# Performance work log

Measured on AMD Instinct MI355X. Metric: run time of the kernel, lower is better.

## Reference

```python
import jax, jax.numpy as jnp
import numpy as np

S = 100        # sos_token_num
H = 12         # num heads
LY = 3         # number of residual blocks
NEG = -100.0   # attention-bias masking value


def layer_norm(x, w, b, eps=1e-5):
    u = jnp.mean(x, -1, keepdims=True)
    v = jnp.mean((x - u) ** 2, -1, keepdims=True)
    return (x - u) / jnp.sqrt(v + eps) * w + b


def quick_gelu(x):
    return x * jax.nn.sigmoid(1.702 * x)


def l2norm(x, eps=1e-12):
    return x / jnp.maximum(jnp.linalg.norm(x, axis=-1, keepdims=True), eps)


def setup_inputs() -> dict:
    key = jax.random.key(0)
    ks = iter(jax.random.split(key, 32))
    n, c, hh, ww, out_dim = 2, 768, 32, 32, 512
    r = lambda shape, s=1.0: jax.random.normal(next(ks), shape, jnp.float32) * s
    return dict(
        cls_token=r((1, n, c)),
        pix_feat=r((n, c, hh, ww)),
        last_surgery=r((1 + hh * ww, n, c)),
        attn_bias=r((n, 1, S, hh, ww)),
        qkv_w=r((LY, 3 * c, c), 0.02), qkv_b=jnp.zeros((LY, 3 * c)),
        proj_w=r((LY, c, c), 0.02), proj_b=jnp.zeros((LY, c)),
        ln1_w=jnp.ones((LY, c)), ln1_b=jnp.zeros((LY, c)),
        ln2_w=jnp.ones((LY, c)), ln2_b=jnp.zeros((LY, c)),
        fc_w=r((LY, 4 * c, c), 0.02), fc_b=jnp.zeros((LY, 4 * c)),
        fc2_w=r((LY, c, 4 * c), 0.02), fc2_b=jnp.zeros((LY, c)),
        lnp_w=jnp.ones((c,)), lnp_b=jnp.zeros((c,)),
        proj_out=r((c, out_dim), 0.02),
    )


def reference(cls_token, pix_feat, last_surgery, attn_bias,
              qkv_w, qkv_b, proj_w, proj_b,
              ln1_w, ln1_b, ln2_w, ln2_b,
              fc_w, fc_b, fc2_w, fc2_b,
              lnp_w, lnp_b, proj_out):
    n, c, hh, ww = pix_feat.shape
    L = hh * ww
    N = S + 1 + L
    d = c // H
    scale = d ** -0.5

    # ---- assemble token streams (batch-first [n, N, c]) ----
    pix_tok = pix_feat.reshape(n, c, L).transpose(2, 0, 1)          # [L, n, c]
    x = jnp.concatenate([jnp.broadcast_to(cls_token, (S, n, c)), cls_token, pix_tok], 0)
    x_sur = jnp.concatenate([jnp.broadcast_to(last_surgery[0:1], (S, n, c)), last_surgery], 0)
    xo = x.transpose(1, 0, 2)      # 'original' stream  [n, N, c]
    xs = x_sur.transpose(1, 0, 2)  # 'surgery'  stream  [n, N, c]

    # ---- build attention biases (identity downsample: bias already at (h, w)) ----
    base = jnp.zeros((N, N), jnp.float32)
    base = base.at[:, :S].set(NEG)
    base = base.at[jnp.arange(S), jnp.arange(S)].set(0.0)
    base = base.at[:S, S].set(NEG)
    plain = jnp.broadcast_to(base, (n, H, N, N))
    bias = jnp.broadcast_to(attn_bias, (n, H, S, hh, ww)).reshape(n, H, S, L)
    biased = plain.at[:, :, :S, S + 1:].set(bias)   # sos rows attend to pixels via bias

    def attention(t, l):
        # t: [n, N, c] (post-ln_1); returns (surgery_res, ori_res)
        qkv = (t @ qkv_w[l].T + qkv_b[l]).reshape(n, N, 3, H, d).transpose(2, 0, 3, 1, 4)
        q, k, v = qkv[0], qkv[1], qkv[2]   # each [n, H, N, d]
        def attend(q_, k_, mask):
            a = jax.nn.softmax(jnp.einsum('bhnd,bhmd->bhnm', q_, k_) * scale + mask, axis=-1)
            o = jnp.einsum('bhnm,bhmd->bhnd', a, v).transpose(0, 2, 1, 3).reshape(n, N, c)
            return o @ proj_w[l].T + proj_b[l]
        x_ori_res = attend(q, k, biased)   # standard pass, biased mask (attn_mask[0])
        x_res = attend(v, v, plain)        # q = k = v surgery pass (attn_mask[1])
        return x_res, x_ori_res

    for l in range(LY):
        t = layer_norm(xo, ln1_w[l], ln1_b[l])
        res_sur, res_ori = attention(t, l)
        xo = xo + res_ori
        xo = xo + (quick_gelu(layer_norm(xo, ln2_w[l], ln2_b[l]) @ fc_w[l].T + fc_b[l]) @ fc2_w[l].T + fc2_b[l])
        xs = xs + res_sur

    # ---- heads ----
    sos = l2norm(layer_norm(xo[:, :S], lnp_w, lnp_b) @ proj_out)          # [n, S, out]
    img = l2norm(layer_norm(xs[:, S:], lnp_w, lnp_b) @ proj_out)          # [n, 1+L, out]
    img = img[:, 1:, :].transpose(0, 2, 1).reshape(n, proj_out.shape[1], hh, ww)
    return sos, img
```

## Files before the change

### kernel.cpp

```cpp
#include <hip/hip_runtime.h>
#include <math.h>


constexpr int Cc = 768;
constexpr int Ss = 100;
constexpr int Hh = 12;
constexpr int Ll = 1024;
constexpr int Nn = 1125;
constexpr int NB = 2;

typedef unsigned short u16;
typedef __attribute__((ext_vector_type(8))) short short8v;
typedef __attribute__((ext_vector_type(8))) unsigned short ushort8v;
typedef __attribute__((ext_vector_type(4))) float f32x4;

__device__ inline u16 f2bf(float f) {
  unsigned u = __builtin_bit_cast(unsigned int, f);
  unsigned r = u + 0x7fffu + ((u >> 16) & 1u);
  return (u16)(r >> 16);
}
__device__ inline float bf2f(u16 v) {
  return __builtin_bit_cast(float, (unsigned int)v << 16);
}

__device__ inline int swz(int row, int col) {
  return (row << 6) + ((((col >> 3) ^ (row & 7)) << 3) | (col & 7));
}

__global__ __launch_bounds__(256) void assemble_kernel(
    const float* __restrict__ cls, const float* __restrict__ pix,
    const float* __restrict__ sur, float* __restrict__ xo, float* __restrict__ xs) {
  int idx = blockIdx.x * 256 + (int)threadIdx.x;
  int total = NB * Nn * Cc;
  if (idx >= total) return;
  int ch = idx % Cc;
  int t  = (idx / Cc) % Nn;
  int b  = idx / (Cc * Nn);
  float vo, vs;
  if (t <= Ss) vo = cls[b * Cc + ch];
  else         vo = pix[(size_t)b * Cc * Ll + (size_t)ch * Ll + (t - Ss - 1)];
  if (t < Ss)  vs = sur[b * Cc + ch];
  else         vs = sur[(size_t)(t - Ss) * NB * Cc + b * Cc + ch];
  xo[idx] = vo;
  xs[idx] = vs;
}

constexpr int CN0 = 3 * 2304 * 768;
constexpr int CN1 = 3 * 768 * 768;
constexpr int CN2 = 3 * 3072 * 768;
constexpr int CN3 = 3 * 768 * 3072;
__global__ __launch_bounds__(256) void cvt4_kernel(
    const float* __restrict__ s0, const float* __restrict__ s1,
    const float* __restrict__ s2, const float* __restrict__ s3,
    u16* __restrict__ dst) {
  int i4 = (blockIdx.x * 256 + (int)threadIdx.x) * 4;
  if (i4 >= CN0 + CN1 + CN2 + CN3) return;
  const float* src; int off;
  if (i4 < CN0)             { src = s0; off = i4; }
  else if (i4 < CN0 + CN1)  { src = s1; off = i4 - CN0; }
  else if (i4 < CN0 + CN1 + CN2) { src = s2; off = i4 - CN0 - CN1; }
  else                      { src = s3; off = i4 - CN0 - CN1 - CN2; }
  float4 v = *(const float4*)(src + off);
  *(ushort4*)(dst + i4) = make_ushort4(f2bf(v.x), f2bf(v.y), f2bf(v.z), f2bf(v.w));
}

__global__ __launch_bounds__(256) void transpose_po_kernel(
    const float* __restrict__ in, u16* __restrict__ out) {
  int id = blockIdx.x * 256 + (int)threadIdx.x;
  if (id >= 512 * 768) return;
  int nidx = id / 768, k = id - nidx * 768;
  out[id] = f2bf(in[(size_t)k * 512 + nidx]);
}

__global__ __launch_bounds__(256) void ln_kernel(
    const float* __restrict__ X, const float* __restrict__ w, const float* __restrict__ b,
    u16* __restrict__ Y, int rows_per_b, int row_off) {
  int r = blockIdx.x;
  int bb = r / rows_per_b;
  int i  = r % rows_per_b;
  const float* x = X + ((size_t)bb * Nn + row_off + i) * Cc;
  u16* y = Y + (size_t)r * Cc;
  int tid = (int)threadIdx.x;
  float v0 = x[tid], v1 = x[tid + 256], v2 = x[tid + 512];
  float s = v0 + v1 + v2;
  __shared__ float sbuf[4];
  for (int off = 32; off; off >>= 1) s += __shfl_xor(s, off);
  if ((tid & 63) == 0) sbuf[tid >> 6] = s;
  __syncthreads();
  float mean = (sbuf[0] + sbuf[1] + sbuf[2] + sbuf[3]) * (1.0f / Cc);
  float d0 = v0 - mean, d1 = v1 - mean, d2 = v2 - mean;
  float q = d0 * d0 + d1 * d1 + d2 * d2;
  __syncthreads();
  for (int off = 32; off; off >>= 1) q += __shfl_xor(q, off);
  if ((tid & 63) == 0) sbuf[tid >> 6] = q;
  __syncthreads();
  float var = (sbuf[0] + sbuf[1] + sbuf[2] + sbuf[3]) * (1.0f / Cc);
  float inv = rsqrtf(var + 1e-5f);
  y[tid]       = f2bf(d0 * inv * w[tid]       + b[tid]);
  y[tid + 256] = f2bf(d1 * inv * w[tid + 256] + b[tid + 256]);
  y[tid + 512] = f2bf(d2 * inv * w[tid + 512] + b[tid + 512]);
}

__global__ __launch_bounds__(256) void gemm64_kernel(
    const u16* __restrict__ A0, const u16* __restrict__ A1,
    const u16* __restrict__ B, const float* __restrict__ bias,
    const float* __restrict__ res0, const float* __restrict__ res1,
    float* __restrict__ outf0, float* __restrict__ outf1,
    u16* __restrict__ outb0, u16* __restrict__ outb1,
    int M, int N, int K, int act) {
  __shared__ __align__(16) u16 Als[64 * 64];
  __shared__ __align__(16) u16 Bls[128 * 64];
  int zz = blockIdx.z;
  const u16* A = zz ? A1 : A0;
  const float* res = zz ? res1 : res0;
  float* outf = zz ? outf1 : outf0;
  u16* outb = zz ? outb1 : outb0;
  int tid = (int)threadIdx.x;
  int wave = tid >> 6, lane = tid & 63, g = lane >> 4, li = lane & 15;
  int row0 = blockIdx.y * 64, col0 = blockIdx.x * 128;

  const u16* aptr[2]; int dA[2];
#pragma unroll
  for (int j = 0; j < 2; ++j) {
    int ca = tid + j * 256;
    int r = ca >> 3, c8 = ca & 7;
    dA[j] = (r << 6) + ((c8 ^ (r & 7)) << 3);
    int ra = row0 + r; if (ra > M - 1) ra = M - 1;
    aptr[j] = A + (size_t)ra * K + (c8 << 3);
  }
  const u16* bptr[4]; int dB[4];
#pragma unroll
  for (int j = 0; j < 4; ++j) {
    int cb = tid + j * 256;
    int r = cb >> 3, c8 = cb & 7;
    dB[j] = (r << 6) + ((c8 ^ (r & 7)) << 3);
    bptr[j] = B + (size_t)(col0 + r) * K + (c8 << 3);
  }

  f32x4 acc[4][2];
#pragma unroll
  for (int mi = 0; mi < 4; ++mi)
#pragma unroll
    for (int ni = 0; ni < 2; ++ni) acc[mi][ni] = (f32x4){0.f, 0.f, 0.f, 0.f};

  for (int k0 = 0; k0 < K; k0 += 64) {
    ushort8v ta[2], tb[4];
#pragma unroll
    for (int j = 0; j < 2; ++j) ta[j] = *(const ushort8v*)(aptr[j] + k0);
#pragma unroll
    for (int j = 0; j < 4; ++j) tb[j] = *(const ushort8v*)(bptr[j] + k0);
    __syncthreads();
#pragma unroll
    for (int j = 0; j < 2; ++j) *(ushort8v*)&Als[dA[j]] = ta[j];
#pragma unroll
    for (int j = 0; j < 4; ++j) *(ushort8v*)&Bls[dB[j]] = tb[j];
    __syncthreads();
#pragma unroll
    for (int kc = 0; kc < 2; ++kc) {
      short8v af[4], bfr[2];
#pragma unroll
      for (int mi = 0; mi < 4; ++mi) {
        int rr = mi * 16 + li;
        af[mi] = *(const short8v*)&Als[(rr << 6) + (((kc * 4 + g) ^ (rr & 7)) << 3)];
      }
#pragma unroll
      for (int ni = 0; ni < 2; ++ni) {
        int rb = wave * 32 + ni * 16 + li;
        bfr[ni] = *(const short8v*)&Bls[(rb << 6) + (((kc * 4 + g) ^ (rb & 7)) << 3)];
      }
#pragma unroll
      for (int mi = 0; mi < 4; ++mi)
#pragma unroll
        for (int ni = 0; ni < 2; ++ni)
          acc[mi][ni] = __builtin_amdgcn_mfma_f32_16x16x32_bf16(af[mi], bfr[ni], acc[mi][ni], 0, 0, 0);
    }
  }

#pragma unroll
  for (int mi = 0; mi < 4; ++mi) {
#pragma unroll
    for (int r = 0; r < 4; ++r) {
      int m = row0 + mi * 16 + g * 4 + r;
      if (m >= M) continue;
#pragma unroll
      for (int ni = 0; ni < 2; ++ni) {
        int n = col0 + wave * 32 + ni * 16 + li;
        float v = acc[mi][ni][r];
        if (bias) v += bias[n];
        if (act)  v = v / (1.0f + __expf(-1.702f * v));
        if (res)  v += res[(size_t)m * N + n];
        if (outf) outf[(size_t)m * N + n] = v;
        else      outb[(size_t)m * N + n] = f2bf(v);
      }
    }
  }
}

__global__ __launch_bounds__(256) void attn_kernel(
    const u16* __restrict__ qkv, const float* __restrict__ abias,
    u16* __restrict__ ao, u16* __restrict__ as_) {
  __shared__ __align__(16) u16 Klds[64 * 64];
  __shared__ __align__(16) u16 Vt[64 * 64];
  __shared__ __align__(16) u16 Plds[4 * 16 * 64];
  int id = (int)blockIdx.x;
  int virt = (id & 7) * 114 + (id >> 3);
  int gid = virt / 19;
  int qt  = virt - gid * 19;
  int z   = gid / 24;
  int bh  = gid - z * 24;
  int b = bh / Hh, h = bh - b * Hh;
  int tid = (int)threadIdx.x;
  int wave = tid >> 6, lane = tid & 63, g = lane >> 4, li = lane & 15;
  bool sosq = qt >= 17;
  u16* outp = z ? as_ : ao;

  int qbase = sosq ? (qt - 17) * 64 + wave * 16 : Ss + qt * 64 + wave * 16;
  int qtok = qbase + li;
  int qcap = sosq ? 99 : 1124;
  if (qtok > qcap) qtok = qcap;
  int qoff = z ? 2 * Cc + h * 64 : h * 64;
  int koff = z ? 2 * Cc + h * 64 : Cc + h * 64;
  int voff = 2 * Cc + h * 64;

  short8v qf[2];
  {
    const u16* qp = qkv + ((size_t)b * Nn + qtok) * 2304 + qoff;
#pragma unroll
    for (int kc = 0; kc < 2; ++kc) {
      ushort8v a = *(const ushort8v*)(qp + kc * 32 + g * 8);
      short8v v;
#pragma unroll
      for (int j = 0; j < 8; ++j) v[j] = (short)f2bf(bf2f(a[j]) * 0.125f);
      qf[kc] = v;
    }
  }

  int skey = tid >> 2;
  int sd0  = (tid & 3) << 4;
  int rot  = tid & 3;
  int kI0 = swz(skey, sd0), kI1 = swz(skey, sd0 + 8);

  f32x4 oacc[4];
#pragma unroll
  for (int nt = 0; nt < 4; ++nt) oacc[nt] = (f32x4){0.f, 0.f, 0.f, 0.f};
  float mrow[4] = {-1e30f, -1e30f, -1e30f, -1e30f};
  float lrow[4] = {0.f, 0.f, 0.f, 0.f};
  int pbase = wave * 1024;

  for (int kt = 0; kt < 17; ++kt) {
    int ktok0 = sosq ? (kt == 0 ? (qt - 17) * 64 : Ss + 1 + (kt - 1) * 64)
                     : Ss + kt * 64;
    __syncthreads();
    {
      int ktok = ktok0 + skey;
      if (ktok <= 1124) {
        const u16* kp = qkv + ((size_t)b * Nn + ktok) * 2304;
        *(ushort8v*)&Klds[kI0] = *(const ushort8v*)(kp + koff + sd0);
        *(ushort8v*)&Klds[kI1] = *(const ushort8v*)(kp + koff + sd0 + 8);
        ushort8v v0 = *(const ushort8v*)(kp + voff + sd0);
        ushort8v v1 = *(const ushort8v*)(kp + voff + sd0 + 8);
        u16 vv[16];
#pragma unroll
        for (int j = 0; j < 8; ++j) { vv[j] = v0[j]; vv[j + 8] = v1[j]; }
#pragma unroll
        for (int mm = 0; mm < 16; ++mm) {
          int jj = (mm + rot) & 15;
          Vt[swz(sd0 + jj, skey)] = vv[jj];
        }
      } else {
        ushort8v zv = (ushort8v)0;
        *(ushort8v*)&Klds[kI0] = zv;
        *(ushort8v*)&Klds[kI1] = zv;
#pragma unroll
        for (int mm = 0; mm < 16; ++mm) Vt[swz(sd0 + mm, skey)] = 0;
      }
    }
    __syncthreads();

    f32x4 sacc[4];
#pragma unroll
    for (int nt = 0; nt < 4; ++nt) sacc[nt] = (f32x4){0.f, 0.f, 0.f, 0.f};
    __builtin_amdgcn_s_setprio(1);
#pragma unroll
    for (int kc = 0; kc < 2; ++kc) {
#pragma unroll
      for (int nt = 0; nt < 4; ++nt) {
        short8v kb = *(const short8v*)&Klds[swz(nt * 16 + li, kc * 32 + g * 8)];
        sacc[nt] = __builtin_amdgcn_mfma_f32_16x16x32_bf16(qf[kc], kb, sacc[nt], 0, 0, 0);
      }
    }
    __builtin_amdgcn_s_setprio(0);

    float rmax[4] = {-1e30f, -1e30f, -1e30f, -1e30f};
    if (!sosq) {
#pragma unroll
      for (int nt = 0; nt < 4; ++nt) {
        int j = ktok0 + nt * 16 + li;
#pragma unroll
        for (int r = 0; r < 4; ++r) {
          float s = (j <= 1124) ? sacc[nt][r] : -1e30f;
          sacc[nt][r] = s;
          rmax[r] = fmaxf(rmax[r], s);
        }
      }
    } else if (kt == 0) {
#pragma unroll
      for (int nt = 0; nt < 4; ++nt) {
        int j = ktok0 + nt * 16 + li;
#pragma unroll
        for (int r = 0; r < 4; ++r) {
          float s = (j == qbase + g * 4 + r) ? sacc[nt][r] : -1e30f;
          sacc[nt][r] = s;
          rmax[r] = fmaxf(rmax[r], s);
        }
      }
    } else if (z == 0) {
#pragma unroll
      for (int nt = 0; nt < 4; ++nt) {
        int j = ktok0 + nt * 16 + li;
#pragma unroll
        for (int r = 0; r < 4; ++r) {
          int i = qbase + g * 4 + r; if (i > 99) i = 99;
          float s = sacc[nt][r] + abias[((size_t)b * Ss + i) * Ll + (j - Ss - 1)];
          sacc[nt][r] = s;
          rmax[r] = fmaxf(rmax[r], s);
        }
      }
    } else {
#pragma unroll
      for (int nt = 0; nt < 4; ++nt)
#pragma unroll
        for (int r = 0; r < 4; ++r) rmax[r] = fmaxf(rmax[r], sacc[nt][r]);
    }

#pragma unroll
    for (int off = 1; off < 16; off <<= 1) {
#pragma unroll
      for (int r = 0; r < 4; ++r) rmax[r] = fmaxf(rmax[r], __shfl_xor(rmax[r], off));
    }
    float fac[4], mnew[4], padd[4];
#pragma unroll
    for (int r = 0; r < 4; ++r) {
      mnew[r] = fmaxf(mrow[r], rmax[r]);
      fac[r] = __expf(mrow[r] - mnew[r]);
      mrow[r] = mnew[r];
      padd[r] = 0.f;
    }
#pragma unroll
    for (int nt = 0; nt < 4; ++nt) {
#pragma unroll
      for (int r = 0; r < 4; ++r) {
        float p = __expf(sacc[nt][r] - mnew[r]);
        padd[r] += p;
        Plds[pbase + swz(g * 4 + r, nt * 16 + li)] = f2bf(p);
      }
    }
#pragma unroll
    for (int r = 0; r < 4; ++r) {
      float ps = padd[r];
#pragma unroll
      for (int off = 1; off < 16; off <<= 1) ps += __shfl_xor(ps, off);
      lrow[r] = lrow[r] * fac[r] + ps;
    }
#pragma unroll
    for (int nt = 0; nt < 4; ++nt) {
#pragma unroll
      for (int r = 0; r < 4; ++r) oacc[nt][r] *= fac[r];
    }

    __builtin_amdgcn_s_setprio(1);
#pragma unroll
    for (int kc = 0; kc < 2; ++kc) {
      short8v pa = *(const short8v*)&Plds[pbase + swz(li, kc * 32 + g * 8)];
#pragma unroll
      for (int nt = 0; nt < 4; ++nt) {
        short8v vb = *(const short8v*)&Vt[swz(nt * 16 + li, kc * 32 + g * 8)];
        oacc[nt] = __builtin_amdgcn_mfma_f32_16x16x32_bf16(pa, vb, oacc[nt], 0, 0, 0);
      }
    }
    __builtin_amdgcn_s_setprio(0);
  }

#pragma unroll
  for (int r = 0; r < 4; ++r) {
    int tok = qbase + g * 4 + r;
    if (tok > qcap) continue;
    float inv = 1.0f / lrow[r];
    u16* op = outp + ((size_t)b * Nn + tok) * Cc + h * 64 + li;
#pragma unroll
    for (int nt = 0; nt < 4; ++nt) op[nt * 16] = f2bf(oacc[nt][r] * inv);
  }
}

__global__ __launch_bounds__(256) void l2norm_sos_kernel(
    const float* __restrict__ Xp, float* __restrict__ out) {
  int r = blockIdx.x;
  int tid = (int)threadIdx.x;
  const float* x = Xp + (size_t)r * 512;
  float v0 = x[tid], v1 = x[tid + 256];
  float s = v0 * v0 + v1 * v1;
  __shared__ float sbuf[4];
  for (int off = 32; off; off >>= 1) s += __shfl_xor(s, off);
  if ((tid & 63) == 0) sbuf[tid >> 6] = s;
  __syncthreads();
  float tot = sbuf[0] + sbuf[1] + sbuf[2] + sbuf[3];
  float inv = 1.0f / fmaxf(sqrtf(tot), 1e-12f);
  out[(size_t)r * 512 + tid]       = v0 * inv;
  out[(size_t)r * 512 + tid + 256] = v1 * inv;
}

__global__ __launch_bounds__(256) void l2norm_img_kernel(
    const float* __restrict__ Xp, float* __restrict__ out) {
  int r = blockIdx.x;
  int b = r / 1025, ti = r % 1025;
  int tid = (int)threadIdx.x;
  const float* x = Xp + (size_t)r * 512;
  float v0 = x[tid], v1 = x[tid + 256];
  float s = v0 * v0 + v1 * v1;
  __shared__ float sbuf[4];
  for (int off = 32; off; off >>= 1) s += __shfl_xor(s, off);
  if ((tid & 63) == 0) sbuf[tid >> 6] = s;
  __syncthreads();
  float tot = sbuf[0] + sbuf[1] + sbuf[2] + sbuf[3];
  if (ti == 0) return;
  float inv = 1.0f / fmaxf(sqrtf(tot), 1e-12f);
  float* o = out + (size_t)b * 512 * 1024 + (ti - 1);
  o[(size_t)tid * 1024]         = v0 * inv;
  o[(size_t)(tid + 256) * 1024] = v1 * inv;
}

extern "C" void kernel_launch(void* const* d_in, const int* in_sizes, int n_in,
                              void* d_out, int out_size, void* d_ws, size_t ws_size,
                              hipStream_t stream) {
  const float* cls      = (const float*)d_in[0];
  const float* pix      = (const float*)d_in[1];
  const float* sur      = (const float*)d_in[2];
  const float* abias    = (const float*)d_in[3];
  const float* qkv_w    = (const float*)d_in[4];
  const float* qkv_b    = (const float*)d_in[5];
  const float* proj_w   = (const float*)d_in[6];
  const float* proj_b   = (const float*)d_in[7];
  const float* ln1_w    = (const float*)d_in[8];
  const float* ln1_b    = (const float*)d_in[9];
  const float* ln2_w    = (const float*)d_in[10];
  const float* ln2_b    = (const float*)d_in[11];
  const float* fc_w     = (const float*)d_in[12];
  const float* fc_b     = (const float*)d_in[13];
  const float* fc2_w    = (const float*)d_in[14];
  const float* fc2_b    = (const float*)d_in[15];
  const float* lnp_w    = (const float*)d_in[16];
  const float* lnp_b    = (const float*)d_in[17];
  const float* proj_o   = (const float*)d_in[18];
  float* out = (float*)d_out;

  const size_t SZ = (size_t)NB * Nn * Cc;
  float* xo      = (float*)d_ws;
  float* xs      = xo + SZ;
  float* head_pj = xs + SZ;
  u16* tln_bf = (u16*)(head_pj + 2250 * 512);
  u16* act_bf = tln_bf + (size_t)2250 * 768;
  u16* ao_bf  = act_bf + (size_t)2250 * 3072;
  u16* as_bf  = ao_bf + (size_t)2250 * 768;
  u16* wq_bf  = as_bf + (size_t)2250 * 768;
  u16* wp_bf  = wq_bf + (size_t)CN0;
  u16* wf_bf  = wp_bf + (size_t)CN1;
  u16* w2_bf  = wf_bf + (size_t)CN2;
  u16* wo_bf  = w2_bf + (size_t)CN3;

  assemble_kernel<<<6750, 256, 0, stream>>>(cls, pix, sur, xo, xs);
  cvt4_kernel<<<20736, 256, 0, stream>>>(qkv_w, proj_w, fc_w, fc2_w, wq_bf);
  transpose_po_kernel<<<1536, 256, 0, stream>>>(proj_o, wo_bf);

  for (int l = 0; l < 3; ++l) {
    ln_kernel<<<2250, 256, 0, stream>>>(xo, ln1_w + l * 768, ln1_b + l * 768, tln_bf, Nn, 0);
    gemm64_kernel<<<dim3(18, 36, 1), 256, 0, stream>>>(
        tln_bf, tln_bf, wq_bf + (size_t)l * 2304 * 768, qkv_b + l * 2304,
        nullptr, nullptr, nullptr, nullptr, act_bf, act_bf, 2250, 2304, 768, 0);
    attn_kernel<<<912, 256, 0, stream>>>(act_bf, abias, ao_bf, as_bf);
    gemm64_kernel<<<dim3(6, 36, 2), 256, 0, stream>>>(
        ao_bf, as_bf, wp_bf + (size_t)l * 768 * 768, proj_b + l * 768,
        xo, xs, xo, xs, nullptr, nullptr, 2250, 768, 768, 0);
    ln_kernel<<<2250, 256, 0, stream>>>(xo, ln2_w + l * 768, ln2_b + l * 768, tln_bf, Nn, 0);
    gemm64_kernel<<<dim3(24, 36, 1), 256, 0, stream>>>(
        tln_bf, tln_bf, wf_bf + (size_t)l * 3072 * 768, fc_b + l * 3072,
        nullptr, nullptr, nullptr, nullptr, act_bf, act_bf, 2250, 3072, 768, 1);
    gemm64_kernel<<<dim3(6, 36, 1), 256, 0, stream>>>(
        act_bf, act_bf, w2_bf + (size_t)l * 768 * 3072, fc2_b + l * 768,
        xo, xo, xo, xo, nullptr, nullptr, 2250, 768, 3072, 0);
  }

  ln_kernel<<<200, 256, 0, stream>>>(xo, lnp_w, lnp_b, tln_bf, 100, 0);
  ln_kernel<<<2050, 256, 0, stream>>>(xs, lnp_w, lnp_b, tln_bf + 200 * 768, 1025, 100);
  gemm64_kernel<<<dim3(4, 36, 1), 256, 0, stream>>>(
      tln_bf, tln_bf, wo_bf, nullptr,
      nullptr, nullptr, head_pj, head_pj, nullptr, nullptr, 2250, 512, 768, 0);
  l2norm_sos_kernel<<<200, 256, 0, stream>>>(head_pj, out);
  l2norm_img_kernel<<<2050, 256, 0, stream>>>(head_pj + 200 * 512, out + 102400);
}
```

Baseline: 923.6 us.

## Transpose attention MFMAs to keep P in registers and use exp2 softmax

Attention now computes S^T by swapping the MFMA operands, so each lane holds one query row. The probabilities then feed the PV MFMA straight from registers through packed bf16 conversion, which removes the LDS round-trip for P. K rows are permuted when stored to LDS so the register layout matches the B operand. Softmax moves to base-2 exp with log2e folded into the Q scale and the bias, and row max/sum reductions drop from 4 shuffle steps per row to 2. Bias loads become float4 and the output is written with packed 8-byte stores, at the cost of more intricate index mapping that could hide correctness errors.

Result: faster. 851.9 us (-7.8%).

```diff
diff --git a/kernel.cpp b/kernel.cpp
--- a/kernel.cpp
+++ b/kernel.cpp
@@ -8,11 +8,14 @@
 constexpr int Ll = 1024;
 constexpr int Nn = 1125;
 constexpr int NB = 2;
+constexpr float QS = 0.18033688011112042f;
+constexpr float LOG2E = 1.4426950408889634f;
 
 typedef unsigned short u16;
 typedef __attribute__((ext_vector_type(8))) short short8v;
 typedef __attribute__((ext_vector_type(8))) unsigned short ushort8v;
 typedef __attribute__((ext_vector_type(4))) float f32x4;
+typedef __attribute__((ext_vector_type(4))) unsigned int u32x4;
 
 __device__ inline u16 f2bf(float f) {
   unsigned u = __builtin_bit_cast(unsigned int, f);
@@ -21,6 +24,11 @@
 }
 __device__ inline float bf2f(u16 v) {
   return __builtin_bit_cast(float, (unsigned int)v << 16);
+}
+__device__ inline unsigned cvtpk(float lo, float hi) {
+  unsigned r;
+  asm("v_cvt_pk_bf16_f32 %0, %1, %2" : "=v"(r) : "v"(lo), "v"(hi));
+  return r;
 }
 
 __device__ inline int swz(int row, int col) {
@@ -201,7 +209,6 @@
     u16* __restrict__ ao, u16* __restrict__ as_) {
   __shared__ __align__(16) u16 Klds[64 * 64];
   __shared__ __align__(16) u16 Vt[64 * 64];
-  __shared__ __align__(16) u16 Plds[4 * 16 * 64];
   int id = (int)blockIdx.x;
   int virt = (id & 7) * 114 + (id >> 3);
   int gid = virt / 19;
@@ -228,24 +235,26 @@
 #pragma unroll
     for (int kc = 0; kc < 2; ++kc) {
       ushort8v a = *(const ushort8v*)(qp + kc * 32 + g * 8);
-      short8v v;
-#pragma unroll
-      for (int j = 0; j < 8; ++j) v[j] = (short)f2bf(bf2f(a[j]) * 0.125f);
-      qf[kc] = v;
+      u32x4 w;
+#pragma unroll
+      for (int jj = 0; jj < 4; ++jj)
+        w[jj] = cvtpk(bf2f(a[2 * jj]) * QS, bf2f(a[2 * jj + 1]) * QS);
+      qf[kc] = __builtin_bit_cast(short8v, w);
     }
   }
 
   int skey = tid >> 2;
   int sd0  = (tid & 3) << 4;
   int rot  = tid & 3;
-  int kI0 = swz(skey, sd0), kI1 = swz(skey, sd0 + 8);
+  int prow = 16 * (2 * (skey >> 5) + ((skey >> 2) & 1)) + 4 * ((skey >> 3) & 3) + (skey & 3);
+  int kI0 = swz(prow, sd0), kI1 = swz(prow, sd0 + 8);
+
+  const int KOFF[4] = {0, 4, 32, 36};
 
   f32x4 oacc[4];
 #pragma unroll
-  for (int nt = 0; nt < 4; ++nt) oacc[nt] = (f32x4){0.f, 0.f, 0.f, 0.f};
-  float mrow[4] = {-1e30f, -1e30f, -1e30f, -1e30f};
-  float lrow[4] = {0.f, 0.f, 0.f, 0.f};
-  int pbase = wave * 1024;
+  for (int dt = 0; dt < 4; ++dt) oacc[dt] = (f32x4){0.f, 0.f, 0.f, 0.f};
+  float mrow = -1e30f, lrow = 0.f;
 
   for (int kt = 0; kt < 17; ++kt) {
     int ktok0 = sosq ? (kt == 0 ? (qt - 17) * 64 : Ss + 1 + (kt - 1) * 64)
@@ -286,109 +295,94 @@
 #pragma unroll
       for (int nt = 0; nt < 4; ++nt) {
         short8v kb = *(const short8v*)&Klds[swz(nt * 16 + li, kc * 32 + g * 8)];
-        sacc[nt] = __builtin_amdgcn_mfma_f32_16x16x32_bf16(qf[kc], kb, sacc[nt], 0, 0, 0);
+        sacc[nt] = __builtin_amdgcn_mfma_f32_16x16x32_bf16(kb, qf[kc], sacc[nt], 0, 0, 0);
       }
     }
     __builtin_amdgcn_s_setprio(0);
 
-    float rmax[4] = {-1e30f, -1e30f, -1e30f, -1e30f};
-    if (!sosq) {
-#pragma unroll
-      for (int nt = 0; nt < 4; ++nt) {
-        int j = ktok0 + nt * 16 + li;
-#pragma unroll
-        for (int r = 0; r < 4; ++r) {
-          float s = (j <= 1124) ? sacc[nt][r] : -1e30f;
-          sacc[nt][r] = s;
-          rmax[r] = fmaxf(rmax[r], s);
+    if (sosq) {
+      if (kt == 0) {
+        int qloc = wave * 16 + li;
+#pragma unroll
+        for (int nt = 0; nt < 4; ++nt)
+#pragma unroll
+          for (int r = 0; r < 4; ++r)
+            if (KOFF[nt] + 8 * g + r != qloc) sacc[nt][r] = -1e30f;
+      } else if (z == 0) {
+        const float* bp = abias + ((size_t)b * Ss + qtok) * Ll + (ktok0 - 101) + 8 * g;
+#pragma unroll
+        for (int nt = 0; nt < 4; ++nt) {
+          float4 bv = *(const float4*)(bp + KOFF[nt]);
+          sacc[nt][0] = fmaf(bv.x, LOG2E, sacc[nt][0]);
+          sacc[nt][1] = fmaf(bv.y, LOG2E, sacc[nt][1]);
+          sacc[nt][2] = fmaf(bv.z, LOG2E, sacc[nt][2]);
+          sacc[nt][3] = fmaf(bv.w, LOG2E, sacc[nt][3]);
         }
       }
-    } else if (kt == 0) {
-#pragma unroll
-      for (int nt = 0; nt < 4; ++nt) {
-        int j = ktok0 + nt * 16 + li;
-#pragma unroll
-        for (int r = 0; r < 4; ++r) {
-          float s = (j == qbase + g * 4 + r) ? sacc[nt][r] : -1e30f;
-          sacc[nt][r] = s;
-          rmax[r] = fmaxf(rmax[r], s);
-        }
-      }
-    } else if (z == 0) {
-#pragma unroll
-      for (int nt = 0; nt < 4; ++nt) {
-        int j = ktok0 + nt * 16 + li;
-#pragma unroll
-        for (int r = 0; r < 4; ++r) {
-          int i = qbase + g * 4 + r; if (i > 99) i = 99;
-          float s = sacc[nt][r] + abias[((size_t)b * Ss + i) * Ll + (j - Ss - 1)];
-          sacc[nt][r] = s;
-          rmax[r] = fmaxf(rmax[r], s);
-        }
-      }
-    } else {
+    } else if (kt == 16) {
 #pragma unroll
       for (int nt = 0; nt < 4; ++nt)
 #pragma unroll
-        for (int r = 0; r < 4; ++r) rmax[r] = fmaxf(rmax[r], sacc[nt][r]);
-    }
-
-#pragma unroll
-    for (int off = 1; off < 16; off <<= 1) {
-#pragma unroll
-      for (int r = 0; r < 4; ++r) rmax[r] = fmaxf(rmax[r], __shfl_xor(rmax[r], off));
-    }
-    float fac[4], mnew[4], padd[4];
-#pragma unroll
-    for (int r = 0; r < 4; ++r) {
-      mnew[r] = fmaxf(mrow[r], rmax[r]);
-      fac[r] = __expf(mrow[r] - mnew[r]);
-      mrow[r] = mnew[r];
-      padd[r] = 0.f;
-    }
-#pragma unroll
-    for (int nt = 0; nt < 4; ++nt) {
+        for (int r = 0; r < 4; ++r)
+          if (ktok0 + KOFF[nt] + 8 * g + r > 1124) sacc[nt][r] = -1e30f;
+    }
+
+    float rmax = -1e30f;
+#pragma unroll
+    for (int nt = 0; nt < 4; ++nt)
+#pragma unroll
+      for (int r = 0; r < 4; ++r) rmax = fmaxf(rmax, sacc[nt][r]);
+    rmax = fmaxf(rmax, __shfl_xor(rmax, 16));
+    rmax = fmaxf(rmax, __shfl_xor(rmax, 32));
+    float mnew = fmaxf(mrow, rmax);
+    float fac = __builtin_amdgcn_exp2f(mrow - mnew);
+    mrow = mnew;
+    float psum = 0.f;
+#pragma unroll
+    for (int nt = 0; nt < 4; ++nt)
 #pragma unroll
       for (int r = 0; r < 4; ++r) {
-        float p = __expf(sacc[nt][r] - mnew[r]);
-        padd[r] += p;
-        Plds[pbase + swz(g * 4 + r, nt * 16 + li)] = f2bf(p);
-      }
-    }
-#pragma unroll
-    for (int r = 0; r < 4; ++r) {
-      float ps = padd[r];
-#pragma unroll
-      for (int off = 1; off < 16; off <<= 1) ps += __shfl_xor(ps, off);
-      lrow[r] = lrow[r] * fac[r] + ps;
-    }
-#pragma unroll
-    for (int nt = 0; nt < 4; ++nt) {
-#pragma unroll
-      for (int r = 0; r < 4; ++r) oacc[nt][r] *= fac[r];
-    }
+        float e = __builtin_amdgcn_exp2f(sacc[nt][r] - mnew);
+        sacc[nt][r] = e;
+        psum += e;
+      }
+    psum += __shfl_xor(psum, 16);
+    psum += __shfl_xor(psum, 32);
+    lrow = lrow * fac + psum;
+#pragma unroll
+    for (int dt = 0; dt < 4; ++dt) oacc[dt] *= fac;
 
     __builtin_amdgcn_s_setprio(1);
 #pragma unroll
-    for (int kc = 0; kc < 2; ++kc) {
-      short8v pa = *(const short8v*)&Plds[pbase + swz(li, kc * 32 + g * 8)];
-#pragma unroll
-      for (int nt = 0; nt < 4; ++nt) {
-        short8v vb = *(const short8v*)&Vt[swz(nt * 16 + li, kc * 32 + g * 8)];
-        oacc[nt] = __builtin_amdgcn_mfma_f32_16x16x32_bf16(pa, vb, oacc[nt], 0, 0, 0);
+    for (int kcp = 0; kcp < 2; ++kcp) {
+      u32x4 pwv;
+#pragma unroll
+      for (int w = 0; w < 4; ++w) {
+        int nt = 2 * kcp + (w >> 1);
+        int r0 = (w & 1) * 2;
+        pwv[w] = cvtpk(sacc[nt][r0], sacc[nt][r0 + 1]);
+      }
+      short8v pb = __builtin_bit_cast(short8v, pwv);
+#pragma unroll
+      for (int dt = 0; dt < 4; ++dt) {
+        short8v va = *(const short8v*)&Vt[swz(dt * 16 + li, kcp * 32 + g * 8)];
+        oacc[dt] = __builtin_amdgcn_mfma_f32_16x16x32_bf16(va, pb, oacc[dt], 0, 0, 0);
       }
     }
     __builtin_amdgcn_s_setprio(0);
   }
 
-#pragma unroll
-  for (int r = 0; r < 4; ++r) {
-    int tok = qbase + g * 4 + r;
-    if (tok > qcap) continue;
-    float inv = 1.0f / lrow[r];
-    u16* op = outp + ((size_t)b * Nn + tok) * Cc + h * 64 + li;
-#pragma unroll
-    for (int nt = 0; nt < 4; ++nt) op[nt * 16] = f2bf(oacc[nt][r] * inv);
+  int tok = qbase + li;
+  if (tok <= qcap) {
+    float inv = 1.0f / lrow;
+    u16* op = outp + ((size_t)b * Nn + tok) * Cc + h * 64 + g * 4;
+#pragma unroll
+    for (int dt = 0; dt < 4; ++dt) {
+      unsigned lo = cvtpk(oacc[dt][0] * inv, oacc[dt][1] * inv);
+      unsigned hi = cvtpk(oacc[dt][2] * inv, oacc[dt][3] * inv);
+      uint2 o2; o2.x = lo; o2.y = hi;
+      *(uint2*)(op + dt * 16) = o2;
+    }
   }
 }
 
```
